# Kernel tuning notes

Hardware: AMD Instinct MI355X
Metric: run time of the kernel (lower is better)

The kernel has to match this reference:

```python
import jax, jax.numpy as jnp
import numpy as np

FEAT_STRIDE = 16
POOL = 7
POST_NMS = 300
NUM_ANCHORS = 9
SCALES = np.array([8.0, 16.0, 32.0])
RATIOS = np.array([0.5, 1.0, 2.0])


def _base_anchors():
    w = h = 16.0
    xc = yc = 7.5
    size = w * h
    ws = np.round(np.sqrt(size / RATIOS))
    hs = np.round(ws * RATIOS)
    ratio_anchors = np.stack([xc - 0.5 * (ws - 1), yc - 0.5 * (hs - 1),
                              xc + 0.5 * (ws - 1), yc + 0.5 * (hs - 1)], 1)
    out = []
    for a in ratio_anchors:
        aw = a[2] - a[0] + 1.0
        ah = a[3] - a[1] + 1.0
        acx = a[0] + 0.5 * (aw - 1)
        acy = a[1] + 0.5 * (ah - 1)
        ws_ = aw * SCALES
        hs_ = ah * SCALES
        out.append(np.stack([acx - 0.5 * (ws_ - 1), acy - 0.5 * (hs_ - 1),
                             acx + 0.5 * (ws_ - 1), acy + 0.5 * (hs_ - 1)], 1))
    return np.concatenate(out, 0)  # [9,4]


def _all_anchors(H, W):
    base = _base_anchors()
    sx = np.arange(W) * FEAT_STRIDE
    sy = np.arange(H) * FEAT_STRIDE
    gx, gy = np.meshgrid(sx, sy)  # [H,W], x fastest -> matches NHWC flatten
    shifts = np.stack([gx.ravel(), gy.ravel(), gx.ravel(), gy.ravel()], 1)
    return jnp.asarray((shifts[:, None, :] + base[None, :, :]).reshape(-1, 4),
                       jnp.float32)  # [H*W*9, 4]


def _conv(x, w, b, pad):
    y = jax.lax.conv_general_dilated(x, w, (1, 1), [(pad, pad), (pad, pad)],
                                     dimension_numbers=('NCHW', 'OIHW', 'NCHW'))
    return y + b[None, :, None, None]


def _affine_grid(theta, H, W):
    # torch affine_grid, align_corners=True (torch<=1.2 default)
    xs = jnp.linspace(-1.0, 1.0, W)
    ys = jnp.linspace(-1.0, 1.0, H)
    gx, gy = jnp.meshgrid(xs, ys)
    base = jnp.stack([gx, gy, jnp.ones_like(gx)], -1)  # [H,W,3]
    return jnp.einsum('nij,hwj->nhwi', theta, base)  # [N,H,W,2] (x,y)


def _bilinear(img, x, y):
    # img [C,H,W]; x,y [h,w] pixel coords; zeros padding, align_corners=True
    H, W = img.shape[1], img.shape[2]
    x0 = jnp.floor(x)
    y0 = jnp.floor(y)
    x1 = x0 + 1.0
    y1 = y0 + 1.0
    wx1 = x - x0
    wx0 = 1.0 - wx1
    wy1 = y - y0
    wy0 = 1.0 - wy1

    def g(xi, yi):
        xc = jnp.clip(xi, 0, W - 1).astype(jnp.int32)
        yc = jnp.clip(yi, 0, H - 1).astype(jnp.int32)
        valid = ((xi >= 0) & (xi <= W - 1) & (yi >= 0) & (yi <= H - 1))
        return img[:, yc, xc] * valid.astype(img.dtype)

    return (g(x0, y0) * (wx0 * wy0) + g(x1, y0) * (wx1 * wy0)
            + g(x0, y1) * (wx0 * wy1) + g(x1, y1) * (wx1 * wy1))


def _pix(grid, H, W):
    x = (grid[..., 0] + 1.0) * 0.5 * (W - 1)
    y = (grid[..., 1] + 1.0) * 0.5 * (H - 1)
    return x, y


def strpn_forward(head_features, im_info, w_rpn, b_rpn, w_cls, b_cls,
                  w_bbox, b_bbox, w_trans, b_trans):
    H, W = head_features.shape[2], head_features.shape[3]
    anchors = _all_anchors(H, W)

    rpn = jax.nn.relu(_conv(head_features, w_rpn, b_rpn, 1))
    cls = _conv(rpn, w_cls, b_cls, 0)      # [1,18,H,W]
    bbox = _conv(rpn, w_bbox, b_bbox, 0)   # [1,36,H,W]
    trans = _conv(rpn, w_trans, b_trans, 0)  # [1,54,H,W]

    # view(1,2,9*H,W) softmax over dim1: channels 0..8=bg, 9..17=fg
    prob = jax.nn.softmax(cls.reshape(1, 2, NUM_ANCHORS, H, W), axis=1)[:, 1]
    scores = prob.transpose(0, 2, 3, 1).reshape(-1)          # [H*W*9]
    deltas = bbox.transpose(0, 2, 3, 1).reshape(-1, 4)
    tparam = trans.transpose(0, 2, 3, 1).reshape(-1, 6)

    # bbox_transform_inv
    aw = anchors[:, 2] - anchors[:, 0] + 1.0
    ah = anchors[:, 3] - anchors[:, 1] + 1.0
    acx = anchors[:, 0] + 0.5 * aw
    acy = anchors[:, 1] + 0.5 * ah
    pcx = deltas[:, 0] * aw + acx
    pcy = deltas[:, 1] * ah + acy
    pw = jnp.exp(deltas[:, 2]) * aw
    ph = jnp.exp(deltas[:, 3]) * ah
    x1 = jnp.clip(pcx - 0.5 * pw, 0.0, im_info[1] - 1.0)
    y1 = jnp.clip(pcy - 0.5 * ph, 0.0, im_info[0] - 1.0)
    x2 = jnp.clip(pcx + 0.5 * pw, 0.0, im_info[1] - 1.0)
    y2 = jnp.clip(pcy + 0.5 * ph, 0.0, im_info[0] - 1.0)

    # proposal selection: fixed-size top-K by fg score (NMS elided, see notes)
    _, idx = jax.lax.top_k(scores, POST_NMS)
    boxes = jnp.stack([x1, y1, x2, y2], 1)[idx]              # [300,4]
    tsel = tparam[idx]                                       # [300,6]
    rois = jnp.concatenate(
        [jnp.zeros((POST_NMS, 1), boxes.dtype), boxes], 1)   # [300,5]

    # affine-grid ROI pooling (STRPN.pooling, max_pool=True)
    fx1 = boxes[:, 0] / 16.0
    fy1 = boxes[:, 1] / 16.0
    fx2 = boxes[:, 2] / 16.0
    fy2 = boxes[:, 3] / 16.0
    Wf = jnp.float32(W)
    Hf = jnp.float32(H)
    t00 = (fx2 - fx1) / (Wf - 1)
    t02 = (fx1 + fx2 - Wf + 1) / (Wf - 1)
    t11 = (fy2 - fy1) / (Hf - 1)
    t12 = (fy1 + fy2 - Hf + 1) / (Hf - 1)
    z = jnp.zeros_like(t00)
    theta = jnp.stack([jnp.stack([t00, z, t02], -1),
                       jnp.stack([z, t11, t12], -1)], 1)     # [300,2,3]

    pre = 2 * POOL
    grid = _affine_grid(theta, pre, pre)
    xg, yg = _pix(grid, H, W)
    img = head_features[0]
    crops = jax.vmap(_bilinear, in_axes=(None, 0, 0))(img, xg, yg)  # [300,C,14,14]
    N, C = crops.shape[0], crops.shape[1]
    pooled = crops.reshape(N, C, POOL, 2, POOL, 2).max(axis=(3, 5))  # [300,C,7,7]

    # spatial transform with predicted per-ROI affine params
    theta2 = tsel.reshape(-1, 2, 3)
    grid2 = _affine_grid(theta2, POOL, POOL)
    x2g, y2g = _pix(grid2, POOL, POOL)
    transformed = jax.vmap(_bilinear)(pooled, x2g, y2g)       # [300,C,7,7]
    return rois, pooled, transformed


def setup_inputs() -> dict:
    key = jax.random.key(0)
    ks = jax.random.split(key, 10)
    C_in, C_rpn = 1024, 512
    inp = {
        'head_features': jax.random.normal(ks[0], (1, C_in, 50, 75), jnp.float32),
        'gt_boxes': jax.random.uniform(ks[1], (5, 5), jnp.float32) * 100.0,
        'im_info': jnp.array([800.0, 1200.0, 1.0], jnp.float32),
        'w_rpn': jax.random.normal(ks[2], (C_rpn, C_in, 3, 3), jnp.float32) * 0.01,
        'b_rpn': jnp.zeros((C_rpn,), jnp.float32),
        'w_cls': jax.random.normal(ks[3], (2 * NUM_ANCHORS, C_rpn, 1, 1), jnp.float32) * 0.01,
        'b_cls': jnp.zeros((2 * NUM_ANCHORS,), jnp.float32),
        'w_bbox': jax.random.normal(ks[4], (4 * NUM_ANCHORS, C_rpn, 1, 1), jnp.float32) * 0.01,
        'b_bbox': jnp.zeros((4 * NUM_ANCHORS,), jnp.float32),
        'w_trans': jax.random.normal(ks[5], (6 * NUM_ANCHORS, C_rpn, 1, 1), jnp.float32) * 0.01,
        'b_trans': jnp.zeros((6 * NUM_ANCHORS,), jnp.float32),
    }
    return inp


def reference(head_features, gt_boxes, im_info, w_rpn, b_rpn, w_cls, b_cls,
              w_bbox, b_bbox, w_trans, b_trans):
    # gt_boxes is unused in the inference 'gallery' path (kept for signature parity)
    return strpn_forward(head_features, im_info, w_rpn, b_rpn, w_cls, b_cls,
                         w_bbox, b_bbox, w_trans, b_trans)
```

## Files before the change

### kernel.cpp

```cpp
#include <hip/hip_runtime.h>
#include <hip/hip_bf16.h>
#include <stdint.h>

typedef unsigned int u32;
typedef unsigned long long u64;

#define HH 50
#define WW 75
#define NPOS 3750
#define NANCH 33750
#define CAP 4096
#define RPSZ 1920000

__constant__ float c_aw[9] = {184.f,368.f,736.f,128.f,256.f,512.f,88.f,176.f,352.f};
__constant__ float c_ah[9] = {96.f,192.f,384.f,128.f,256.f,512.f,176.f,352.f,704.f};

__global__ __launch_bounds__(256) void k_tw2(const float* __restrict__ w, float* __restrict__ wTb) {
  __shared__ __align__(16) float T[72*129];
  int tile = blockIdx.x;
  int ch   = blockIdx.y;
  int ocb = tile >> 2, ks = tile & 3;
  int t = threadIdx.x;
  const float* src = w + (size_t)(ocb*128)*9216 + (size_t)(ks*256 + ch*8)*9;
  #pragma unroll
  for (int i = 0; i < 36; ++i) {
    int e = t + i*256;
    int oc = e / 72, f = e - oc*72;
    T[f*129 + oc] = src[(size_t)oc*9216 + f];
  }
  __syncthreads();
  float* dst = wTb + ((size_t)tile*32 + ch)*9216;
  #pragma unroll
  for (int i = 0; i < 9; ++i) {
    int j = t + i*256;
    int f = j >> 5, o4 = (j & 31)*4;
    float4 v = make_float4(T[f*129+o4], T[f*129+o4+1], T[f*129+o4+2], T[f*129+o4+3]);
    *(float4*)&dst[(size_t)j*4] = v;
  }
}

__global__ __launch_bounds__(256) void k_pad2(const float* __restrict__ head, float* __restrict__ hp) {
  int T = blockIdx.x*256 + threadIdx.x;
  int ic = T / 1218; int rem = T - ic*1218;
  int r = rem / 21, c4 = rem - r*21;
  int sy = r - 1;
  float v[4];
  #pragma unroll
  for (int c = 0; c < 4; ++c) {
    int sx = c4*4 + c - 1;
    v[c] = (sy >= 0 && sy < HH && sx >= 0 && sx < WW)
         ? head[(size_t)ic*NPOS + sy*WW + sx] : 0.f;
  }
  *(float4*)&hp[(size_t)T*4] = make_float4(v[0],v[1],v[2],v[3]);
}

__global__ __launch_bounds__(256) void k_tf(const float* __restrict__ head, float* __restrict__ fT) {
  __shared__ float tile[32][33];
  int p0 = blockIdx.x*32, c0 = blockIdx.y*32;
  int tx = threadIdx.x & 31, ty = threadIdx.x >> 5;
  #pragma unroll
  for (int k = 0; k < 4; ++k) {
    int cc = c0 + ty + k*8, pp = p0 + tx;
    tile[ty + k*8][tx] = (pp < NPOS) ? head[(size_t)cc*NPOS + pp] : 0.f;
  }
  __syncthreads();
  #pragma unroll
  for (int k = 0; k < 4; ++k) {
    int pp = p0 + ty + k*8, cc = c0 + tx;
    if (pp < NPOS) fT[(size_t)pp*1024 + cc] = tile[tx][ty + k*8];
  }
}

__global__ __launch_bounds__(256) void k_conv(const float* __restrict__ hp,
                                              const float* __restrict__ wTb,
                                              float* __restrict__ rpnP) {
  __shared__ __align__(16) float Xs[2][1600];
  int ocb = blockIdx.x;
  int ks  = blockIdx.z;
  int g   = blockIdx.y;
  int R   = g / 5, sub = g - (g/5)*5;
  int t = threadIdx.x;
  int w = t >> 6, lane = t & 63;
  int or0 = __builtin_amdgcn_readfirstlane(8*R + 2*w);
  bool awave = (or0 < HH);
  int rloc = __builtin_amdgcn_readfirstlane(2*w);
  int x0 = sub*16;

  const float* wsrc = wTb + (size_t)(ocb*4 + ks)*32*9216 + 2*lane;
  int ic0 = ks*256;

  int f1 = t + 256;
  bool has1 = f1 < 400;
  int il0 = t/50,  r0 = (t%50)/5,  x40 = t%5;
  int il1 = f1/50, r1 = (f1%50)/5, x41 = f1%5;
  const float4* hp4 = (const float4*)hp;
  size_t c0s = (size_t)(ic0 + il0)*1218 + (size_t)(8*R + r0)*21 + 4*sub + x40;
  size_t c1s = (size_t)(ic0 + il1)*1218 + (size_t)(8*R + r1)*21 + 4*sub + x41;

  float4 s0 = hp4[c0s];
  float4 s1 = has1 ? hp4[c1s] : s0;
  ((float4*)Xs[0])[t] = s0;
  if (has1) ((float4*)Xs[0])[f1] = s1;
  __syncthreads();

  float a00[16], a01[16], a10[16], a11[16];
  #pragma unroll
  for (int j = 0; j < 16; ++j) { a00[j]=0.f; a01[j]=0.f; a10[j]=0.f; a11[j]=0.f; }

  #pragma unroll 1
  for (int ch = 0; ch < 32; ++ch) {
    int cur = ch & 1;
    if (ch < 31) {
      size_t adv = (size_t)(ch+1)*8*1218;
      s0 = hp4[c0s + adv];
      if (has1) s1 = hp4[c1s + adv];
    }
    if (awave) {
      const float* wch = wsrc + (size_t)ch*9216;
      #pragma unroll 1
      for (int il = 0; il < 8; ++il) {
        float wv0[9], wv1[9];
        #pragma unroll
        for (int k = 0; k < 9; ++k) {
          float2 w2 = *(const float2*)(wch + (il*9 + k)*128);
          wv0[k] = w2.x; wv1[k] = w2.y;
        }
        const float* xb = &Xs[cur][il*200 + rloc*20 + x0/4*4];
        #pragma unroll
        for (int ri = 0; ri < 4; ++ri) {
          const float* xr = &Xs[cur][il*200 + (rloc + ri)*20];
          float4 q0 = *(const float4*)(xr + 0);
          float4 q1 = *(const float4*)(xr + 4);
          float4 q2 = *(const float4*)(xr + 8);
          float4 q3 = *(const float4*)(xr + 12);
          float4 q4 = *(const float4*)(xr + 16);
          float xv[20] = {q0.x,q0.y,q0.z,q0.w, q1.x,q1.y,q1.z,q1.w,
                          q2.x,q2.y,q2.z,q2.w, q3.x,q3.y,q3.z,q3.w,
                          q4.x,q4.y,q4.z,q4.w};
          if (ri < 3) {
            #pragma unroll
            for (int kx = 0; kx < 3; ++kx) {
              float w0 = wv0[ri*3+kx], w1 = wv1[ri*3+kx];
              #pragma unroll
              for (int j = 0; j < 16; ++j) {
                a00[j] = fmaf(w0, xv[j+kx], a00[j]);
                a01[j] = fmaf(w1, xv[j+kx], a01[j]);
              }
            }
          }
          if (ri > 0) {
            #pragma unroll
            for (int kx = 0; kx < 3; ++kx) {
              float w0 = wv0[(ri-1)*3+kx], w1 = wv1[(ri-1)*3+kx];
              #pragma unroll
              for (int j = 0; j < 16; ++j) {
                a10[j] = fmaf(w0, xv[j+kx], a10[j]);
                a11[j] = fmaf(w1, xv[j+kx], a11[j]);
              }
            }
          }
        }
      }
    }
    if (ch < 31) {
      ((float4*)Xs[cur^1])[t] = s0;
      if (has1) ((float4*)Xs[cur^1])[f1] = s1;
    }
    __syncthreads();
  }

  if (awave) {
    float* outp = rpnP + (size_t)ks*RPSZ;
    int ocl = ocb*128 + 2*lane;
    #pragma unroll
    for (int j = 0; j < 16; ++j) {
      int x = x0 + j;
      if (x < WW) {
        *(float2*)&outp[(size_t)(or0*WW + x)*512 + ocl]       = make_float2(a00[j], a01[j]);
        *(float2*)&outp[(size_t)((or0+1)*WW + x)*512 + ocl]   = make_float2(a10[j], a11[j]);
      }
    }
  }
}

__global__ __launch_bounds__(256) void k_cls(const float* __restrict__ rp,
    const float* __restrict__ brpn,
    const float* __restrict__ w_cls, const float* __restrict__ b_cls,
    const float* __restrict__ w_bbox, const float* __restrict__ b_bbox,
    const float* __restrict__ w_tr, const float* __restrict__ b_tr,
    const float* __restrict__ iminfo,
    u32* __restrict__ sk, float* __restrict__ boxes, float* __restrict__ tpar) {
  __shared__ __align__(16) float R[128*68];
  __shared__ float O[16][112];
  int p0 = blockIdx.x << 4;
  int t = threadIdx.x;
  for (int e = t; e < 8192; e += 256) {
    int pos = e >> 9, ic = e & 511;
    int p = p0 + pos;
    float v = 0.f;
    if (p < NPOS) {
      size_t off = (size_t)p*512 + ic;
      v = rp[off] + rp[off + RPSZ] + rp[off + 2*(size_t)RPSZ] + rp[off + 3*(size_t)RPSZ] + brpn[ic];
      v = fmaxf(v, 0.f);
    }
    R[(ic>>2)*68 + pos*4 + (ic&3)] = v;
  }
  __syncthreads();
  int og = t >> 4, pos = t & 15;
  float acc[7];
  const float* wp[7];
  #pragma unroll
  for (int k = 0; k < 7; ++k) {
    acc[k] = 0.f;
    int o = og + (k << 4);
    if (o < 18)       wp[k] = w_cls + (size_t)o*512;
    else if (o < 54)  wp[k] = w_bbox + (size_t)(o-18)*512;
    else if (o < 108) wp[k] = w_tr + (size_t)(o-54)*512;
    else              wp[k] = w_cls;
  }
  for (int icg = 0; icg < 128; ++icg) {
    float4 xv = *(const float4*)&R[icg*68 + pos*4];
    #pragma unroll
    for (int k = 0; k < 7; ++k) {
      float4 wv = *(const float4*)(wp[k] + icg*4);
      acc[k] = fmaf(xv.x, wv.x, acc[k]);
      acc[k] = fmaf(xv.y, wv.y, acc[k]);
      acc[k] = fmaf(xv.z, wv.z, acc[k]);
      acc[k] = fmaf(xv.w, wv.w, acc[k]);
    }
  }
  #pragma unroll
  for (int k = 0; k < 7; ++k) {
    int o = og + (k << 4);
    if (o < 108) {
      float bv = (o < 18) ? b_cls[o] : (o < 54) ? b_bbox[o-18] : b_tr[o-54];
      O[pos][o] = acc[k] + bv;
    }
  }
  __syncthreads();
  if (t < 144) {
    int ps = t / 9, a = t - ps*9;
    int p = p0 + ps;
    if (p < NPOS) {
      int i = p*9 + a;
      float d = O[ps][9+a] - O[ps][a];
      float prob = 1.f / (1.f + expf(-d));
      u32 u = __float_as_uint(prob);
      sk[i] = (u & 0x80000000u) ? ~u : (u | 0x80000000u);
      int y = p / WW, x = p - y*WW;
      float aw = c_aw[a], ah = c_ah[a];
      float acx = x*16.f + 8.f, acy = y*16.f + 8.f;
      float dx = O[ps][18+a*4], dyv = O[ps][18+a*4+1], dz = O[ps][18+a*4+2], dw = O[ps][18+a*4+3];
      float pcx = dx*aw + acx, pcy = dyv*ah + acy;
      float pw = expf(dz)*aw, ph = expf(dw)*ah;
      float imh = iminfo[0], imw = iminfo[1];
      float x1 = fminf(fmaxf(pcx - 0.5f*pw, 0.f), imw - 1.f);
      float y1 = fminf(fmaxf(pcy - 0.5f*ph, 0.f), imh - 1.f);
      float x2 = fminf(fmaxf(pcx + 0.5f*pw, 0.f), imw - 1.f);
      float y2 = fminf(fmaxf(pcy + 0.5f*ph, 0.f), imh - 1.f);
      *(float4*)(boxes + (size_t)i*4) = make_float4(x1,y1,x2,y2);
      #pragma unroll
      for (int j = 0; j < 6; ++j) tpar[(size_t)i*6 + j] = O[ps][54 + a*6 + j];
    }
  }
}

__global__ __launch_bounds__(256) void k_hist(const u32* __restrict__ sk, u32* __restrict__ hist) {
  int i = blockIdx.x*256 + threadIdx.x;
  if (i < NANCH) atomicAdd(&hist[sk[i] >> 16], 1u);
}

__global__ __launch_bounds__(1024) void k_thresh(const u32* __restrict__ hist, u32* __restrict__ thr) {
  __shared__ u32 S[1024];
  __shared__ int tstar;
  int t = threadIdx.x;
  u32 s = 0;
  for (int j = 0; j < 64; ++j) s += hist[t*64 + j];
  S[t] = s;
  __syncthreads();
  for (int d = 1; d < 1024; d <<= 1) {
    u32 v = (t + d < 1024) ? S[t + d] : 0;
    __syncthreads();
    S[t] += v;
    __syncthreads();
  }
  if (S[t] >= 300 && (t == 1023 || S[t+1] < 300)) tstar = t;
  __syncthreads();
  if (t == 0) {
    int ts = tstar;
    u32 c = (ts < 1023) ? S[ts+1] : 0;
    int T = ts*64;
    for (int b = ts*64 + 63; b >= ts*64; --b) {
      c += hist[b];
      if (c >= 300) { T = b; break; }
    }
    thr[0] = (u32)T;
  }
}

__global__ __launch_bounds__(256) void k_compact(const u32* __restrict__ sk, const u32* __restrict__ thr,
                                                 u64* __restrict__ cand, u32* __restrict__ cnt) {
  int i = blockIdx.x*256 + threadIdx.x;
  if (i >= NANCH) return;
  u32 k = sk[i];
  if ((k >> 16) >= thr[0]) {
    u32 p = atomicAdd(cnt, 1u);
    if (p < CAP) cand[p] = ((u64)k << 32) | (u32)(~(u32)i);
  }
}

__global__ __launch_bounds__(1024) void k_sortsel(const u64* __restrict__ cand, const u32* __restrict__ cnt,
    const float* __restrict__ boxes, const float* __restrict__ tpar,
    float* __restrict__ out_rois, float* __restrict__ selb, float* __restrict__ selt) {
  __shared__ u64 A[CAP];
  int t = threadIdx.x;
  int n = min((int)cnt[0], CAP);
  for (int i = t; i < CAP; i += 1024) A[i] = (i < n) ? cand[i] : 0ull;
  __syncthreads();
  for (int k = 2; k <= CAP; k <<= 1) {
    for (int j = k >> 1; j > 0; j >>= 1) {
      for (int i = t; i < CAP; i += 1024) {
        int p = i ^ j;
        if (p > i) {
          u64 a = A[i], b = A[p];
          bool dir = (i & k) == 0;
          if (dir ? (a < b) : (a > b)) { A[i] = b; A[p] = a; }
        }
      }
      __syncthreads();
    }
  }
  if (t < 300) {
    u32 idx = ~((u32)A[t]);
    float4 bx = *(const float4*)(boxes + (size_t)idx*4);
    out_rois[t*5+0] = 0.f;
    out_rois[t*5+1] = bx.x; out_rois[t*5+2] = bx.y;
    out_rois[t*5+3] = bx.z; out_rois[t*5+4] = bx.w;
    *(float4*)(selb + t*4) = bx;
    #pragma unroll
    for (int j = 0; j < 6; ++j) selt[t*6+j] = tpar[(size_t)idx*6 + j];
  }
}

__global__ __launch_bounds__(256) void k_pool(const float* __restrict__ fT,
    const float* __restrict__ selb, const float* __restrict__ selt,
    float* __restrict__ outP, float* __restrict__ outTr) {
  __shared__ __align__(16) float pl[256*49];
  int r = blockIdx.y;
  int c0 = blockIdx.x << 8;
  int t = threadIdx.x;
  const float* img = fT + c0 + t;
  float bx1 = selb[r*4], by1 = selb[r*4+1], bx2 = selb[r*4+2], by2 = selb[r*4+3];
  float fx1 = bx1*0.0625f, fy1 = by1*0.0625f, fx2 = bx2*0.0625f, fy2 = by2*0.0625f;
  float t00 = (fx2-fx1)*(1.f/74.f);
  float t02 = (fx1+fx2-74.f)*(1.f/74.f);
  float t11 = (fy2-fy1)*(1.f/49.f);
  float t12 = (fy1+fy2-49.f)*(1.f/49.f);
  for (int py = 0; py < 7; ++py) {
    float m[7];
    #pragma unroll
    for (int q = 0; q < 7; ++q) m[q] = -3.4e38f;
    #pragma unroll
    for (int dy = 0; dy < 2; ++dy) {
      int sy = py*2 + dy;
      float gy = -1.f + sy*(2.f/13.f);
      float yf = (t11*gy + t12 + 1.f)*24.5f;
      float y0f = floorf(yf);
      float wy1 = yf - y0f, wy0 = 1.f - wy1;
      bool vy0 = (y0f >= 0.f && y0f <= 49.f);
      bool vy1 = (y0f >= -1.f && y0f <= 48.f);
      float yc = fminf(fmaxf(y0f, -2.f), 51.f);
      int iy0 = min(max((int)yc, 0), 49);
      int iy1 = min(max((int)yc + 1, 0), 49);
      #pragma unroll
      for (int sx = 0; sx < 14; ++sx) {
        float gx = -1.f + sx*(2.f/13.f);
        float xf = (t00*gx + t02 + 1.f)*37.f;
        float x0f = floorf(xf);
        float wx1 = xf - x0f, wx0 = 1.f - wx1;
        bool vx0 = (x0f >= 0.f && x0f <= 74.f);
        bool vx1 = (x0f >= -1.f && x0f <= 73.f);
        float xc = fminf(fmaxf(x0f, -2.f), 76.f);
        int ix0 = min(max((int)xc, 0), 74);
        int ix1 = min(max((int)xc + 1, 0), 74);
        float v00 = (vx0 && vy0) ? img[(size_t)(iy0*WW + ix0)*1024] : 0.f;
        float v10 = (vx1 && vy0) ? img[(size_t)(iy0*WW + ix1)*1024] : 0.f;
        float v01 = (vx0 && vy1) ? img[(size_t)(iy1*WW + ix0)*1024] : 0.f;
        float v11 = (vx1 && vy1) ? img[(size_t)(iy1*WW + ix1)*1024] : 0.f;
        float val = v00*(wx0*wy0) + v10*(wx1*wy0) + v01*(wx0*wy1) + v11*(wx1*wy1);
        m[sx>>1] = fmaxf(m[sx>>1], val);
      }
    }
    #pragma unroll
    for (int q = 0; q < 7; ++q) pl[t*49 + py*7 + q] = m[q];
  }
  __syncthreads();
  size_t base = (size_t)r*50176 + (size_t)c0*49;
  for (int jj = t; jj < 3136; jj += 256)
    *(float4*)(outP + base + (size_t)jj*4) = *(const float4*)&pl[jj*4];
  float T0 = selt[r*6], T1 = selt[r*6+1], T2 = selt[r*6+2];
  float T3 = selt[r*6+3], T4 = selt[r*6+4], T5 = selt[r*6+5];
  float tr[49];
  #pragma unroll
  for (int qy = 0; qy < 7; ++qy) {
    float gy = -1.f + qy*(1.f/3.f);
    #pragma unroll
    for (int qx = 0; qx < 7; ++qx) {
      float gx = -1.f + qx*(1.f/3.f);
      float xf = (T0*gx + T1*gy + T2 + 1.f)*3.f;
      float yf = (T3*gx + T4*gy + T5 + 1.f)*3.f;
      float x0f = floorf(xf), y0f = floorf(yf);
      float wx1 = xf - x0f, wx0 = 1.f - wx1;
      float wy1 = yf - y0f, wy0 = 1.f - wy1;
      bool vx0 = (x0f >= 0.f && x0f <= 6.f), vx1 = (x0f >= -1.f && x0f <= 5.f);
      bool vy0 = (y0f >= 0.f && y0f <= 6.f), vy1 = (y0f >= -1.f && y0f <= 5.f);
      float xc = fminf(fmaxf(x0f, -2.f), 8.f);
      float ycl = fminf(fmaxf(y0f, -2.f), 8.f);
      int ix0 = min(max((int)xc, 0), 6), ix1 = min(max((int)xc + 1, 0), 6);
      int iy0 = min(max((int)ycl, 0), 6), iy1 = min(max((int)ycl + 1, 0), 6);
      const float* P = &pl[t*49];
      float v00 = (vx0&&vy0) ? P[iy0*7+ix0] : 0.f;
      float v10 = (vx1&&vy0) ? P[iy0*7+ix1] : 0.f;
      float v01 = (vx0&&vy1) ? P[iy1*7+ix0] : 0.f;
      float v11 = (vx1&&vy1) ? P[iy1*7+ix1] : 0.f;
      tr[qy*7+qx] = v00*(wx0*wy0) + v10*(wx1*wy0) + v01*(wx0*wy1) + v11*(wx1*wy1);
    }
  }
  __syncthreads();
  #pragma unroll
  for (int q = 0; q < 49; ++q) pl[t*49 + q] = tr[q];
  __syncthreads();
  for (int jj = t; jj < 3136; jj += 256)
    *(float4*)(outTr + base + (size_t)jj*4) = *(const float4*)&pl[jj*4];
}

extern "C" void kernel_launch(void* const* d_in, const int* in_sizes, int n_in,
                              void* d_out, int out_size, void* d_ws, size_t ws_size,
                              hipStream_t stream) {
  (void)in_sizes; (void)n_in; (void)out_size; (void)ws_size;
  const float* head   = (const float*)d_in[0];
  const float* iminfo = (const float*)d_in[2];
  const float* w_rpn  = (const float*)d_in[3];
  const float* b_rpn  = (const float*)d_in[4];
  const float* w_cls  = (const float*)d_in[5];
  const float* b_cls  = (const float*)d_in[6];
  const float* w_bbox = (const float*)d_in[7];
  const float* b_bbox = (const float*)d_in[8];
  const float* w_tr   = (const float*)d_in[9];
  const float* b_tr   = (const float*)d_in[10];
  float* out = (float*)d_out;
  float* out_rois = out;
  float* outP = out + 1500;
  float* outT = out + 1500 + 15052800;

  char* wsp = (char*)d_ws;
  size_t off = 0;
  auto alloc = [&](size_t bytes) -> void* {
    void* p = wsp + off;
    off = (off + bytes + 255) & ~(size_t)255;
    return p;
  };
  float* wTb   = (float*)alloc(4718592ull*4);
  float* hp    = (float*)alloc(4988928ull*4);
  float* rpnP  = (float*)alloc(4ull*RPSZ*4);
  u32*   sk    = (u32*)alloc(NANCH*4);
  float* boxes = (float*)alloc((size_t)NANCH*4*4);
  float* tpar  = (float*)alloc((size_t)NANCH*6*4);
  u32*   hist  = (u32*)alloc(65536*4);
  u32*   cnt   = (u32*)alloc(256);
  u64*   cand  = (u64*)alloc(CAP*8);
  float* selb  = (float*)alloc(300*4*4);
  float* selt  = (float*)alloc(300*6*4);
  float* fT    = hp;

  hipMemsetAsync(hist, 0, 65536*4, stream);
  hipMemsetAsync(cnt, 0, 8, stream);

  k_tw2<<<dim3(16, 32), 256, 0, stream>>>(w_rpn, wTb);
  k_pad2<<<4872, 256, 0, stream>>>(head, hp);
  k_conv<<<dim3(4, 35, 4), 256, 0, stream>>>(hp, wTb, rpnP);
  k_tf<<<dim3(118, 32), 256, 0, stream>>>(head, fT);
  k_cls<<<235, 256, 0, stream>>>(rpnP, b_rpn, w_cls, b_cls, w_bbox, b_bbox,
                                 w_tr, b_tr, iminfo, sk, boxes, tpar);
  k_hist<<<132, 256, 0, stream>>>(sk, hist);
  k_thresh<<<1, 1024, 0, stream>>>(hist, cnt + 1);
  k_compact<<<132, 256, 0, stream>>>(sk, cnt + 1, cand, cnt);
  k_sortsel<<<1, 1024, 0, stream>>>(cand, cnt, boxes, tpar, out_rois, selb, selt);
  k_pool<<<dim3(4, 300), 256, 0, stream>>>(fT, selb, selt, outP, outT);
}
```

Measured before the change: 1.120 ms.

## Fuse weight transpose into conv via LDS staging and split-K across eight slices

Drops the separate weight-transpose kernel. The conv kernel now stages the 128-output-channel weight slice for each 4-input-channel chunk into shared memory directly from the original weight layout. The spatial tiling is reorganised so each wave handles one 2-row by 16-column tile, and blocks are packed so all waves have work. Split-K goes from 4 to 8 slices, which doubles the partial-sum buffer and the reads in the classifier kernel. The input is no longer double-buffered, so global loads now sit between two barriers on every chunk.

```diff
diff --git a/kernel.cpp b/kernel.cpp
--- a/kernel.cpp
+++ b/kernel.cpp
@@ -15,30 +15,6 @@
 __constant__ float c_aw[9] = {184.f,368.f,736.f,128.f,256.f,512.f,88.f,176.f,352.f};
 __constant__ float c_ah[9] = {96.f,192.f,384.f,128.f,256.f,512.f,176.f,352.f,704.f};
 
-__global__ __launch_bounds__(256) void k_tw2(const float* __restrict__ w, float* __restrict__ wTb) {
-  __shared__ __align__(16) float T[72*129];
-  int tile = blockIdx.x;
-  int ch   = blockIdx.y;
-  int ocb = tile >> 2, ks = tile & 3;
-  int t = threadIdx.x;
-  const float* src = w + (size_t)(ocb*128)*9216 + (size_t)(ks*256 + ch*8)*9;
-  #pragma unroll
-  for (int i = 0; i < 36; ++i) {
-    int e = t + i*256;
-    int oc = e / 72, f = e - oc*72;
-    T[f*129 + oc] = src[(size_t)oc*9216 + f];
-  }
-  __syncthreads();
-  float* dst = wTb + ((size_t)tile*32 + ch)*9216;
-  #pragma unroll
-  for (int i = 0; i < 9; ++i) {
-    int j = t + i*256;
-    int f = j >> 5, o4 = (j & 31)*4;
-    float4 v = make_float4(T[f*129+o4], T[f*129+o4+1], T[f*129+o4+2], T[f*129+o4+3]);
-    *(float4*)&dst[(size_t)j*4] = v;
-  }
-}
-
 __global__ __launch_bounds__(256) void k_pad2(const float* __restrict__ head, float* __restrict__ hp) {
   int T = blockIdx.x*256 + threadIdx.x;
   int ic = T / 1218; int rem = T - ic*1218;
@@ -72,36 +48,31 @@
 }
 
 __global__ __launch_bounds__(256) void k_conv(const float* __restrict__ hp,
-                                              const float* __restrict__ wTb,
+                                              const float* __restrict__ w_rpn,
                                               float* __restrict__ rpnP) {
-  __shared__ __align__(16) float Xs[2][1600];
+  __shared__ __align__(16) float Ws[36*130];
+  __shared__ __align__(16) float Xs[4*6*84];
   int ocb = blockIdx.x;
   int ks  = blockIdx.z;
-  int g   = blockIdx.y;
-  int R   = g / 5, sub = g - (g/5)*5;
   int t = threadIdx.x;
   int w = t >> 6, lane = t & 63;
-  int or0 = __builtin_amdgcn_readfirstlane(8*R + 2*w);
-  bool awave = (or0 < HH);
-  int rloc = __builtin_amdgcn_readfirstlane(2*w);
+  int gw = blockIdx.y*4 + w;
+  int g = gw < 125 ? gw : 124;
+  int rp  = __builtin_amdgcn_readfirstlane(g / 5);
+  int sub = __builtin_amdgcn_readfirstlane(g - (g/5)*5);
+  int rpA = __builtin_amdgcn_readfirstlane((int)((blockIdx.y*4) / 5));
+  int rloc = 2*(rp - rpA);
   int x0 = sub*16;
 
-  const float* wsrc = wTb + (size_t)(ocb*4 + ks)*32*9216 + 2*lane;
-  int ic0 = ks*256;
-
-  int f1 = t + 256;
-  bool has1 = f1 < 400;
-  int il0 = t/50,  r0 = (t%50)/5,  x40 = t%5;
-  int il1 = f1/50, r1 = (f1%50)/5, x41 = f1%5;
   const float4* hp4 = (const float4*)hp;
-  size_t c0s = (size_t)(ic0 + il0)*1218 + (size_t)(8*R + r0)*21 + 4*sub + x40;
-  size_t c1s = (size_t)(ic0 + il1)*1218 + (size_t)(8*R + r1)*21 + 4*sub + x41;
-
-  float4 s0 = hp4[c0s];
-  float4 s1 = has1 ? hp4[c1s] : s0;
-  ((float4*)Xs[0])[t] = s0;
-  if (has1) ((float4*)Xs[0])[f1] = s1;
-  __syncthreads();
+  const float* wbase = w_rpn + (size_t)(ocb*128)*9216 + (size_t)(ks*128)*9;
+
+  int e0 = t, e1 = t + 256;
+  int il0 = e0/126, r0 = (e0%126)/21, c40 = e0%21;
+  int il1 = e1/126, r1 = (e1%126)/21, c41 = e1%21;
+  bool has1 = e1 < 504;
+  size_t xa0 = (size_t)(ks*128 + il0)*1218 + (size_t)(2*rpA + r0)*21 + c40;
+  size_t xa1 = (size_t)(ks*128 + il1)*1218 + (size_t)(2*rpA + r1)*21 + c41;
 
   float a00[16], a01[16], a10[16], a11[16];
   #pragma unroll
@@ -109,76 +80,73 @@
 
   #pragma unroll 1
   for (int ch = 0; ch < 32; ++ch) {
-    int cur = ch & 1;
-    if (ch < 31) {
-      size_t adv = (size_t)(ch+1)*8*1218;
-      s0 = hp4[c0s + adv];
-      if (has1) s1 = hp4[c1s + adv];
-    }
-    if (awave) {
-      const float* wch = wsrc + (size_t)ch*9216;
-      #pragma unroll 1
-      for (int il = 0; il < 8; ++il) {
-        float wv0[9], wv1[9];
-        #pragma unroll
-        for (int k = 0; k < 9; ++k) {
-          float2 w2 = *(const float2*)(wch + (il*9 + k)*128);
-          wv0[k] = w2.x; wv1[k] = w2.y;
-        }
-        const float* xb = &Xs[cur][il*200 + rloc*20 + x0/4*4];
-        #pragma unroll
-        for (int ri = 0; ri < 4; ++ri) {
-          const float* xr = &Xs[cur][il*200 + (rloc + ri)*20];
-          float4 q0 = *(const float4*)(xr + 0);
-          float4 q1 = *(const float4*)(xr + 4);
-          float4 q2 = *(const float4*)(xr + 8);
-          float4 q3 = *(const float4*)(xr + 12);
-          float4 q4 = *(const float4*)(xr + 16);
-          float xv[20] = {q0.x,q0.y,q0.z,q0.w, q1.x,q1.y,q1.z,q1.w,
-                          q2.x,q2.y,q2.z,q2.w, q3.x,q3.y,q3.z,q3.w,
-                          q4.x,q4.y,q4.z,q4.w};
-          if (ri < 3) {
+    const float* wc = wbase + (size_t)ch*36;
+    #pragma unroll
+    for (int i = 0; i < 18; ++i) {
+      int e = t + i*256;
+      int oc = e / 36, f = e - oc*36;
+      Ws[f*130 + oc] = wc[(size_t)oc*9216 + f];
+    }
+    size_t adv = (size_t)ch*(4*1218);
+    ((float4*)Xs)[e0] = hp4[xa0 + adv];
+    if (has1) ((float4*)Xs)[e1] = hp4[xa1 + adv];
+    __syncthreads();
+    #pragma unroll 1
+    for (int il = 0; il < 4; ++il) {
+      float wv0[9], wv1[9];
+      #pragma unroll
+      for (int k = 0; k < 9; ++k) {
+        float2 w2 = *(const float2*)&Ws[(il*9 + k)*130 + 2*lane];
+        wv0[k] = w2.x; wv1[k] = w2.y;
+      }
+      const float* xb = &Xs[il*504 + rloc*84 + x0];
+      #pragma unroll
+      for (int ri = 0; ri < 4; ++ri) {
+        const float* xr = xb + ri*84;
+        float4 q0 = *(const float4*)(xr + 0);
+        float4 q1 = *(const float4*)(xr + 4);
+        float4 q2 = *(const float4*)(xr + 8);
+        float4 q3 = *(const float4*)(xr + 12);
+        float4 q4 = *(const float4*)(xr + 16);
+        float xv[20] = {q0.x,q0.y,q0.z,q0.w, q1.x,q1.y,q1.z,q1.w,
+                        q2.x,q2.y,q2.z,q2.w, q3.x,q3.y,q3.z,q3.w,
+                        q4.x,q4.y,q4.z,q4.w};
+        if (ri < 3) {
+          #pragma unroll
+          for (int kx = 0; kx < 3; ++kx) {
+            float w0 = wv0[ri*3+kx], w1 = wv1[ri*3+kx];
             #pragma unroll
-            for (int kx = 0; kx < 3; ++kx) {
-              float w0 = wv0[ri*3+kx], w1 = wv1[ri*3+kx];
-              #pragma unroll
-              for (int j = 0; j < 16; ++j) {
-                a00[j] = fmaf(w0, xv[j+kx], a00[j]);
-                a01[j] = fmaf(w1, xv[j+kx], a01[j]);
-              }
+            for (int j = 0; j < 16; ++j) {
+              a00[j] = fmaf(w0, xv[j+kx], a00[j]);
+              a01[j] = fmaf(w1, xv[j+kx], a01[j]);
             }
           }
-          if (ri > 0) {
+        }
+        if (ri > 0) {
+          #pragma unroll
+          for (int kx = 0; kx < 3; ++kx) {
+            float w0 = wv0[(ri-1)*3+kx], w1 = wv1[(ri-1)*3+kx];
             #pragma unroll
-            for (int kx = 0; kx < 3; ++kx) {
-              float w0 = wv0[(ri-1)*3+kx], w1 = wv1[(ri-1)*3+kx];
-              #pragma unroll
-              for (int j = 0; j < 16; ++j) {
-                a10[j] = fmaf(w0, xv[j+kx], a10[j]);
-                a11[j] = fmaf(w1, xv[j+kx], a11[j]);
-              }
+            for (int j = 0; j < 16; ++j) {
+              a10[j] = fmaf(w0, xv[j+kx], a10[j]);
+              a11[j] = fmaf(w1, xv[j+kx], a11[j]);
             }
           }
         }
       }
     }
-    if (ch < 31) {
-      ((float4*)Xs[cur^1])[t] = s0;
-      if (has1) ((float4*)Xs[cur^1])[f1] = s1;
-    }
     __syncthreads();
   }
 
-  if (awave) {
-    float* outp = rpnP + (size_t)ks*RPSZ;
-    int ocl = ocb*128 + 2*lane;
-    #pragma unroll
-    for (int j = 0; j < 16; ++j) {
-      int x = x0 + j;
-      if (x < WW) {
-        *(float2*)&outp[(size_t)(or0*WW + x)*512 + ocl]       = make_float2(a00[j], a01[j]);
-        *(float2*)&outp[(size_t)((or0+1)*WW + x)*512 + ocl]   = make_float2(a10[j], a11[j]);
-      }
+  float* outp = rpnP + (size_t)ks*RPSZ;
+  int ocl = ocb*128 + 2*lane;
+  int or0 = 2*rp;
+  #pragma unroll
+  for (int j = 0; j < 16; ++j) {
+    int x = x0 + j;
+    if (x < WW) {
+      *(float2*)&outp[(size_t)(or0*WW + x)*512 + ocl]     = make_float2(a00[j], a01[j]);
+      *(float2*)&outp[(size_t)((or0+1)*WW + x)*512 + ocl] = make_float2(a10[j], a11[j]);
     }
   }
 }
@@ -200,7 +168,9 @@
     float v = 0.f;
     if (p < NPOS) {
       size_t off = (size_t)p*512 + ic;
-      v = rp[off] + rp[off + RPSZ] + rp[off + 2*(size_t)RPSZ] + rp[off + 3*(size_t)RPSZ] + brpn[ic];
+      v = brpn[ic];
+      #pragma unroll
+      for (int q = 0; q < 8; ++q) v += rp[off + (size_t)q*RPSZ];
       v = fmaxf(v, 0.f);
     }
     R[(ic>>2)*68 + pos*4 + (ic&3)] = v;
@@ -460,9 +430,8 @@
     off = (off + bytes + 255) & ~(size_t)255;
     return p;
   };
-  float* wTb   = (float*)alloc(4718592ull*4);
   float* hp    = (float*)alloc(4988928ull*4);
-  float* rpnP  = (float*)alloc(4ull*RPSZ*4);
+  float* rpnP  = (float*)alloc(8ull*RPSZ*4);
   u32*   sk    = (u32*)alloc(NANCH*4);
   float* boxes = (float*)alloc((size_t)NANCH*4*4);
   float* tpar  = (float*)alloc((size_t)NANCH*6*4);
@@ -476,9 +445,8 @@
   hipMemsetAsync(hist, 0, 65536*4, stream);
   hipMemsetAsync(cnt, 0, 8, stream);
 
-  k_tw2<<<dim3(16, 32), 256, 0, stream>>>(w_rpn, wTb);
   k_pad2<<<4872, 256, 0, stream>>>(head, hp);
-  k_conv<<<dim3(4, 35, 4), 256, 0, stream>>>(hp, wTb, rpnP);
+  k_conv<<<dim3(4, 32, 8), 256, 0, stream>>>(hp, w_rpn, rpnP);
   k_tf<<<dim3(118, 32), 256, 0, stream>>>(head, fT);
   k_cls<<<235, 256, 0, stream>>>(rpnP, b_rpn, w_cls, b_cls, w_bbox, b_bbox,
                                  w_tr, b_tr, iminfo, sk, boxes, tpar);
```

Result: slower. 1.855 ms (+65.6%).
